# Optimization experiments

Hardware: AMD Instinct MI355X
Metric: run time of the kernel (lower is better)

Reference implementation:

```python
import jax, jax.numpy as jnp
import numpy as np

NP = 4            # num_patches
P = NP * NP       # num_patches^2
BIG = 1e8         # self-distance sentinel used by the torch module
IN_CH = 128
MID = IN_CH // 2
NUM_CONVS = 3
KS = 3
B, H, W = 4, 256, 256


def conv2d(x, w, b):
    # x: [B,C,H,W], w: [O,I,kh,kw] (OIHW), stride 1, 'same' padding
    pad = (w.shape[-1] - 1) // 2
    y = jax.lax.conv_general_dilated(
        x, w, window_strides=(1, 1), padding=[(pad, pad), (pad, pad)],
        dimension_numbers=('NCHW', 'OIHW', 'NCHW'))
    return y + b[None, :, None, None]


def patchify(x):
    # [B,C,H,W] -> [B,P,C,hs,ws] with row-major patch order (i*NP+j)
    b, c, h, w = x.shape
    hs, ws = h // NP, w // NP
    x = x.reshape(b, c, NP, hs, NP, ws).transpose(0, 2, 4, 1, 3, 5)
    return x.reshape(b, P, c, hs, ws)


def unpatchify(xp, h, w):
    b, p, c, hs, ws = xp.shape
    x = xp.reshape(b, NP, NP, c, hs, ws).transpose(0, 3, 1, 4, 2, 5)
    return x.reshape(b, c, h, w)


def setup_inputs() -> dict:
    key = jax.random.key(0)
    ks = jax.random.split(key, 16)
    s = 0.05  # weight init scale (~kaiming for these fan-ins)
    inp = {
        'x':     jax.random.normal(ks[0], (B, IN_CH, H, W), jnp.float32),
        'pre_w': jax.random.normal(ks[1], (MID, IN_CH, KS, KS), jnp.float32) * s,
        'pre_b': jnp.zeros((MID,), jnp.float32),
        'c1_w':  jax.random.normal(ks[2], (NUM_CONVS, MID, MID, KS, KS), jnp.float32) * s,
        'c1_b':  jnp.zeros((NUM_CONVS, MID), jnp.float32),
        'c2_w':  jax.random.normal(ks[3], (NUM_CONVS, MID, MID, KS, KS), jnp.float32) * s,
        'c2_b':  jnp.zeros((NUM_CONVS, MID), jnp.float32),
        'p1_w':  jax.random.normal(ks[4], (P, MID, MID), jnp.float32) * s,  # [patch, out, in] 1x1 conv
        'p1_b':  jnp.zeros((P, MID), jnp.float32),
        'p2_w':  jax.random.normal(ks[5], (P, MID, MID), jnp.float32) * s,
        'p2_b':  jnp.zeros((P, MID), jnp.float32),
        'fin_w': jax.random.normal(ks[6], (IN_CH, IN_CH, KS, KS), jnp.float32) * s,
        'fin_b': jnp.zeros((IN_CH,), jnp.float32),
    }
    return inp


def reference(x, pre_w, pre_b, c1_w, c1_b, c2_w, c2_b,
              p1_w, p1_b, p2_w, p2_b, fin_w, fin_b):
    x0 = jax.nn.relu(conv2d(x, pre_w, pre_b))
    h1 = x0
    for i in range(c1_w.shape[0]):
        h1 = jax.nn.relu(conv2d(h1, c1_w[i], c1_b[i]))
    x1 = h1 + x0
    h2 = x0
    for i in range(c2_w.shape[0]):
        h2 = jax.nn.relu(conv2d(h2, c2_w[i], c2_b[i]))
    x2 = h2 + x0

    # per-patch 1x1 convs (all P patches batched via einsum)
    x1p = patchify(x1)  # [B,P,C,hs,ws]
    x2p = patchify(x2)
    x1p = jnp.einsum('bpchw,pdc->bpdhw', x1p, p1_w) + p1_b[None, :, :, None, None]
    x2p = jnp.einsum('bpchw,pdc->bpdhw', x2p, p2_w) + p2_b[None, :, :, None, None]

    # pairwise squared distances between x1 patches and x2 patches
    f1 = x1p.reshape(B, P, -1)
    f2 = x2p.reshape(B, P, -1)
    d = ((f1 ** 2).sum(-1)[:, :, None]
         + (f2 ** 2).sum(-1)[:, None, :]
         - 2.0 * jnp.einsum('bpd,bqd->bpq', f1, f2))  # [B,P,P]
    d = jnp.where(jnp.eye(P, dtype=bool)[None], BIG, d)
    # torch does softmax(exp(-d)) — keep the double transform faithfully
    attn = jax.nn.softmax(jnp.exp(-d), axis=-1)  # [B,P,P]

    outp = jnp.einsum('bpq,bqchw->bpchw', attn, x2p)
    out = unpatchify(outp, H, W)           # [B,MID,H,W]
    out = jnp.concatenate([out, x0], axis=1)  # [B,IN_CH,H,W]
    out = jax.nn.relu(conv2d(out, fin_w, fin_b))
    return out + x
```

## Files before the change

### kernel.cpp

```cpp
#include <hip/hip_runtime.h>
#include <hip/hip_bf16.h>

#define BB   4
#define HH   256
#define WW   256
#define INCH 128
#define MIDC 64
#define NPAT 4
#define PP   16
#define PS   64

typedef __bf16 bf16x8 __attribute__((ext_vector_type(8)));
typedef float f32x4 __attribute__((ext_vector_type(4)));
typedef unsigned short ushort_t;

#define UPL 16777216UL

__device__ inline ushort_t f2bf(float f) {
    unsigned u = __float_as_uint(f);
    unsigned r = (u + 0x7FFFu + ((u >> 16) & 1u)) >> 16;
    return (ushort_t)r;
}
__device__ inline float bf2f(ushort_t h) {
    return __uint_as_float(((unsigned)h) << 16);
}
__device__ inline f32x4 mfma16(uint4 a, uint4 b, f32x4 c) {
    return __builtin_amdgcn_mfma_f32_16x16x32_bf16(
        __builtin_bit_cast(bf16x8, a), __builtin_bit_cast(bf16x8, b), c, 0, 0, 0);
}

__global__ __launch_bounds__(256) void setup_kernel(
    const float* __restrict__ x,     ushort_t* __restrict__ xh,
    const float* __restrict__ pre_w, const float* __restrict__ c1_w,
    const float* __restrict__ c2_w,  const float* __restrict__ fin_w,
    const float* __restrict__ p1_w,  const float* __restrict__ p2_w,
    const float* __restrict__ c1_b,  const float* __restrict__ c2_b,
    ushort_t* __restrict__ wpPre, ushort_t* __restrict__ wpC,
    ushort_t* __restrict__ wpFin, ushort_t* __restrict__ pw1b,
    ushort_t* __restrict__ pw2b,  float* __restrict__ zbuf,
    float* __restrict__ cbias)
{
    __shared__ ushort_t sm[64 * 136];
    const int t = threadIdx.x;
    const int bx = blockIdx.x;
    if (bx < 4096) {
        const int b = bx >> 10;
        const int pxbase = (bx & 1023) * 64;
#pragma unroll
        for (int i = 0; i < 32; ++i) {
            int idx = i * 256 + t;
            int c = idx >> 6, pxl = idx & 63;
            sm[pxl * 136 + c] = f2bf(x[((size_t)(b * 128 + c)) * 65536 + pxbase + pxl]);
        }
        __syncthreads();
#pragma unroll
        for (int i = 0; i < 4; ++i) {
            int idx = i * 256 + t;
            int pxl = idx >> 4, q = idx & 15;
            uint4 v = *(const uint4*)&sm[pxl * 136 + q * 8];
            *(uint4*)(xh + ((size_t)b * 65536 + pxbase + pxl) * 128 + q * 8) = v;
        }
        return;
    }
    int idx = (bx - 4096) * 256 + t;
    if (idx < 73728) {
        int tap = idx % 9, ci = (idx / 9) % 128, co = idx / 1152;
        wpPre[(tap * 64 + co) * 128 + ci] = f2bf(pre_w[idx]);
    } else if (idx < 294912) {
        int j = idx - 73728;
        int which = j / 36864, k = j % 36864;
        const float* src = (which < 3) ? (c1_w + (size_t)which * 36864)
                                       : (c2_w + (size_t)(which - 3) * 36864);
        int tap = k % 9, ci = (k / 9) % 64, co = k / 576;
        wpC[(size_t)which * 36864 + (tap * 64 + co) * 64 + ci] = f2bf(src[k]);
    } else if (idx < 442368) {
        int k = idx - 294912;
        int tap = k % 9, ci = (k / 9) % 128, co = k / 1152;
        wpFin[(tap * 128 + co) * 128 + ci] = f2bf(fin_w[k]);
    } else if (idx < 507904) {
        pw1b[idx - 442368] = f2bf(p1_w[idx - 442368]);
    } else if (idx < 573440) {
        pw2b[idx - 507904] = f2bf(p2_w[idx - 507904]);
    } else if (idx < 574592) {
        zbuf[idx - 573440] = 0.f;
    } else if (idx < 574784) {
        cbias[idx - 574592] = c1_b[idx - 574592];
    } else if (idx < 574976) {
        cbias[192 + idx - 574784] = c2_b[idx - 574784];
    }
}

template<int CIN, int CSPLIT>
__device__ inline void stage10x34(const ushort_t* inA, const ushort_t* inB,
                                  int b, int y0, int x0, int t, int cb,
                                  uint4 (&stg)[6])
{
#pragma unroll
    for (int i = 0; i < 6; ++i) {
        int e = i * 256 + t;
        int pxl = e >> 2, quad = e & 3;
        int row = pxl / 34, xl = pxl - row * 34;
        int gy = y0 + row - 1, gx = x0 + xl - 1;
        bool ok = (e < 1360) && ((unsigned)gy < 256u) && ((unsigned)gx < 256u);
        int c0 = cb + quad * 8;
        const ushort_t* src; int nch, ch;
        if ((CSPLIT == CIN) || (c0 < CSPLIT)) { src = inA; nch = CSPLIT; ch = c0; }
        else { src = inB; nch = CIN - CSPLIT; ch = c0 - CSPLIT; }
        uint4 v = make_uint4(0u, 0u, 0u, 0u);
        if (ok) v = *(const uint4*)(src + ((size_t)((b * 256 + gy) * 256 + gx)) * nch + ch);
        stg[i] = v;
    }
}

template<int CIN, int CSPLIT>
__device__ inline void stage6x68(const ushort_t* inA, const ushort_t* inB,
                                 int b, int y0, int x0, int t, int cb,
                                 uint4 (&stg)[7])
{
#pragma unroll
    for (int i = 0; i < 7; ++i) {
        int e = i * 256 + t;
        int pxl = e >> 2, quad = e & 3;
        int row = pxl / 68, xl = pxl - row * 68;
        int gy = y0 + row - 1, gx = x0 + xl - 1;
        bool ok = (e < 1632) && ((unsigned)gy < 256u) && ((unsigned)gx < 256u);
        int c0 = cb + quad * 8;
        const ushort_t* src; int nch, ch;
        if ((CSPLIT == CIN) || (c0 < CSPLIT)) { src = inA; nch = CSPLIT; ch = c0; }
        else { src = inB; nch = CIN - CSPLIT; ch = c0 - CSPLIT; }
        uint4 v = make_uint4(0u, 0u, 0u, 0u);
        if (ok) v = *(const uint4*)(src + ((size_t)((b * 256 + gy) * 256 + gx)) * nch + ch);
        stg[i] = v;
    }
}

template<int CIN, int CSPLIT, int OMODE, bool PAIR>
__global__ __launch_bounds__(256) void mconv3x3(
    const ushort_t* __restrict__ inA, const ushort_t* __restrict__ inB,
    const ushort_t* __restrict__ wgtT,
    const float* __restrict__ bias,
    const void* __restrict__ res,
    void* __restrict__ out,
    int COUT, size_t inStride, size_t wStride, size_t bStride, size_t outStride)
{
    constexpr int NCH = CIN / 32;
    __shared__ ushort_t sm[10 * 34 * 36];

    const int t = threadIdx.x;
    const int nx = gridDim.x;
    const int bid = blockIdx.x;
    const int fid = (bid & 7) * (nx >> 3) + (bid >> 3);
    const int tile = fid;
    const int cog = PAIR ? 0 : blockIdx.y * 64;
    const int y0 = (tile >> 3) * 8;
    const int x0 = (tile & 7) * 32;
    const int br = PAIR ? blockIdx.y : 0;
    const ushort_t* inAb = inA + (size_t)br * inStride;
    const ushort_t* inBb = inB + (size_t)br * inStride;
    const ushort_t* wgt  = wgtT + (size_t)br * wStride;
    const float*    bs   = bias + (size_t)br * bStride;
    const int b = blockIdx.z;
    const int l = t & 63, w = t >> 6;
    const int lan15 = l & 15;
    const int g4 = l >> 4;
    const int k8 = g4 * 8;
    const int co0 = cog + (w & 1) * 32;
    const int xw = (w >> 1) * 16;

    f32x4 acc[2][8];
#pragma unroll
    for (int mt = 0; mt < 2; ++mt)
#pragma unroll
        for (int r = 0; r < 8; ++r) acc[mt][r] = (f32x4)0.f;

    uint4 stg[6];
    stage10x34<CIN, CSPLIT>(inAb, inBb, b, y0, x0, t, 0, stg);

    for (int cc = 0; cc < NCH; ++cc) {
        __syncthreads();
#pragma unroll
        for (int i = 0; i < 6; ++i) {
            int e = i * 256 + t;
            if (e < 1360) {
                int pxl = e >> 2, quad = e & 3;
                *(uint4*)&sm[pxl * 36 + quad * 8] = stg[i];
            }
        }
        __syncthreads();
        if (cc + 1 < NCH)
            stage10x34<CIN, CSPLIT>(inAb, inBb, b, y0, x0, t, (cc + 1) * 32, stg);

        const int cb = cc * 32;
        uint4 af[2][9];
#pragma unroll
        for (int mt = 0; mt < 2; ++mt)
#pragma unroll
            for (int tap = 0; tap < 9; ++tap)
                af[mt][tap] = *(const uint4*)(wgt +
                    ((size_t)tap * COUT + co0 + mt * 16 + lan15) * CIN + cb + k8);

#pragma unroll
        for (int s = 0; s < 10; ++s) {
#pragma unroll
            for (int dx = 0; dx < 3; ++dx) {
                const int pxl = s * 34 + xw + lan15 + dx;
                uint4 bv = *(const uint4*)&sm[pxl * 36 + k8];
#pragma unroll
                for (int dy = 0; dy < 3; ++dy) {
                    const int r = s - dy;
                    if (r >= 0 && r < 8) {
                        acc[0][r] = mfma16(af[0][dy * 3 + dx], bv, acc[0][r]);
                        acc[1][r] = mfma16(af[1][dy * 3 + dx], bv, acc[1][r]);
                    }
                }
            }
        }
    }

#pragma unroll
    for (int mt = 0; mt < 2; ++mt) {
#pragma unroll
        for (int r = 0; r < 8; ++r) {
            const int y = y0 + r;
            const int x = x0 + xw + lan15;
            const int codr = co0 + mt * 16 + g4 * 4;
            float v[4];
#pragma unroll
            for (int j = 0; j < 4; ++j)
                v[j] = fmaxf(acc[mt][r][j] + bs[codr + j], 0.f);
            const size_t pix = (size_t)(b * 256 + y) * 256 + x;
            if constexpr (OMODE == 1) {
                const ushort_t* rp = (const ushort_t*)res + pix * 64 + codr;
#pragma unroll
                for (int j = 0; j < 4; ++j) v[j] += bf2f(rp[j]);
            }
            uint2 pk;
            pk.x = (unsigned)f2bf(v[0]) | ((unsigned)f2bf(v[1]) << 16);
            pk.y = (unsigned)f2bf(v[2]) | ((unsigned)f2bf(v[3]) << 16);
            *(uint2*)((ushort_t*)out + (size_t)br * outStride + pix * COUT + codr) = pk;
        }
    }
}

template<int CIN, int CSPLIT, int OMODE, bool COPAIR>
__global__ __launch_bounds__(256) void wconv3x3(
    const ushort_t* __restrict__ inA, const ushort_t* __restrict__ inB,
    const ushort_t* __restrict__ wgtT,
    const float* __restrict__ bias,
    const void* __restrict__ res,
    void* __restrict__ out,
    int COUT)
{
    constexpr int NCH = CIN / 32;
    __shared__ ushort_t sm[6 * 68 * 32];

    const int t = threadIdx.x;
    const int nx = gridDim.x;
    const int bid = blockIdx.x;
    const int fid = (bid & 7) * (nx >> 3) + (bid >> 3);
    int tile, cog;
    if (COPAIR) { tile = fid >> 1; cog = (fid & 1) * 64; }
    else        { tile = fid;      cog = blockIdx.y * 64; }
    const int y0 = (tile >> 2) * 4;
    const int x0 = (tile & 3) * 64;
    const int b = blockIdx.z;
    const int l = t & 63, w = t >> 6;
    const int lan15 = l & 15;
    const int g4 = l >> 4;
    const int k8 = g4 * 8;
    const int co0 = cog + (w & 1) * 32;
    const int wrow0 = (w >> 1) * 2;

    f32x4 acc[2][8];
#pragma unroll
    for (int mt = 0; mt < 2; ++mt)
#pragma unroll
        for (int nt = 0; nt < 8; ++nt) acc[mt][nt] = (f32x4)0.f;

    uint4 stg[7];
    stage6x68<CIN, CSPLIT>(inA, inB, b, y0, x0, t, 0, stg);

    for (int cc = 0; cc < NCH; ++cc) {
        __syncthreads();
#pragma unroll
        for (int i = 0; i < 7; ++i) {
            int e = i * 256 + t;
            if (e < 1632) {
                int pxl = e >> 2, quad = e & 3;
                *(uint4*)&sm[pxl * 32 + quad * 8] = stg[i];
            }
        }
        __syncthreads();
        if (cc + 1 < NCH)
            stage6x68<CIN, CSPLIT>(inA, inB, b, y0, x0, t, (cc + 1) * 32, stg);

        const int cb = cc * 32;
        uint4 af[2][9];
#pragma unroll
        for (int mt = 0; mt < 2; ++mt)
#pragma unroll
            for (int tap = 0; tap < 9; ++tap)
                af[mt][tap] = *(const uint4*)(wgtT +
                    ((size_t)tap * COUT + co0 + mt * 16 + lan15) * CIN + cb + k8);

#pragma unroll
        for (int rr = 0; rr < 4; ++rr) {
            const int r = wrow0 + rr;
#pragma unroll
            for (int col = 0; col < 4; ++col) {
#pragma unroll
                for (int dx = 0; dx < 3; ++dx) {
                    const int xc = col * 16 + lan15 + dx;
                    uint4 bv = *(const uint4*)&sm[(r * 68 + xc) * 32 + k8];
#pragma unroll
                    for (int drow = 0; drow < 2; ++drow) {
                        const int dy = rr - drow;
                        if (dy >= 0 && dy < 3) {
                            const int tap = dy * 3 + dx;
                            const int nt = drow * 4 + col;
                            acc[0][nt] = mfma16(af[0][tap], bv, acc[0][nt]);
                            acc[1][nt] = mfma16(af[1][tap], bv, acc[1][nt]);
                        }
                    }
                }
            }
        }
    }

#pragma unroll
    for (int mt = 0; mt < 2; ++mt) {
#pragma unroll
        for (int nt = 0; nt < 8; ++nt) {
            const int y = y0 + wrow0 + (nt >> 2);
            const int x = x0 + (nt & 3) * 16 + lan15;
            const int codr = co0 + mt * 16 + g4 * 4;
            float v[4];
#pragma unroll
            for (int j = 0; j < 4; ++j)
                v[j] = fmaxf(acc[mt][nt][j] + bias[codr + j], 0.f);
            if constexpr (OMODE == 2) {
                const float* rf = (const float*)res;
                float* of = (float*)out;
#pragma unroll
                for (int j = 0; j < 4; ++j) {
                    size_t oi = ((size_t)(b * COUT + codr + j) * 256 + y) * 256 + x;
                    of[oi] = v[j] + rf[oi];
                }
            } else {
                const size_t pix = (size_t)(b * 256 + y) * 256 + x;
                uint2 pk;
                pk.x = (unsigned)f2bf(v[0]) | ((unsigned)f2bf(v[1]) << 16);
                pk.y = (unsigned)f2bf(v[2]) | ((unsigned)f2bf(v[3]) << 16);
                *(uint2*)((ushort_t*)out + pix * COUT + codr) = pk;
            }
        }
    }
}

__global__ __launch_bounds__(256) void patch1x1_mfma(
    const ushort_t* __restrict__ in0, const ushort_t* __restrict__ pwb0,
    const float* __restrict__ bias1, const float* __restrict__ bias2,
    ushort_t* __restrict__ outp0, float* __restrict__ nrm0)
{
    __shared__ ushort_t smp[256 * 72];
    const int side = blockIdx.z;
    const ushort_t* in  = in0  + (size_t)side * UPL;
    const ushort_t* pwb = pwb0 + side * 65536;
    const float*   bias = side ? bias2 : bias1;
    ushort_t*      outp = outp0 + (size_t)side * UPL;
    float*         nrm  = nrm0 + side * 64;

    const int t = threadIdx.x;
    const int bx = blockIdx.x;
    const int bp = blockIdx.y;
    const int b = bp >> 4, p = bp & 15;
    const int py = (p >> 2) * 64, px0 = (p & 3) * 64;
    const int l = t & 63, w = t >> 6;
    const int lan15 = l & 15, k8 = (l >> 4) * 8;

#pragma unroll
    for (int i = 0; i < 8; ++i) {
        int idx = i * 256 + t;
        int px = idx >> 3, q = idx & 7;
        int y = py + bx * 4 + (px >> 6), x = px0 + (px & 63);
        uint4 v = *(const uint4*)(in + ((size_t)(b * 256 + y) * 256 + x) * 64 + q * 8);
        *(uint4*)&smp[px * 72 + q * 8] = v;
    }
    __syncthreads();

    uint4 af[4][2];
#pragma unroll
    for (int mt = 0; mt < 4; ++mt)
#pragma unroll
        for (int kk = 0; kk < 2; ++kk)
            af[mt][kk] = *(const uint4*)(pwb + (size_t)p * 4096 +
                                         (mt * 16 + lan15) * 64 + kk * 32 + k8);

    f32x4 acc[4][4];
#pragma unroll
    for (int mt = 0; mt < 4; ++mt)
#pragma unroll
        for (int j = 0; j < 4; ++j) acc[mt][j] = (f32x4)0.f;

#pragma unroll
    for (int kk = 0; kk < 2; ++kk)
#pragma unroll
        for (int j = 0; j < 4; ++j) {
            int px = (w * 4 + j) * 16 + lan15;
            uint4 bv = *(const uint4*)&smp[px * 72 + kk * 32 + k8];
#pragma unroll
            for (int mt = 0; mt < 4; ++mt)
                acc[mt][j] = mfma16(af[mt][kk], bv, acc[mt][j]);
        }

    float nsum = 0.f;
#pragma unroll
    for (int mt = 0; mt < 4; ++mt)
#pragma unroll
        for (int j = 0; j < 4; ++j) {
            int px = (w * 4 + j) * 16 + lan15;
            int y = py + bx * 4 + (px >> 6), x = px0 + (px & 63);
            int d0 = mt * 16 + (l >> 4) * 4;
            float v[4];
#pragma unroll
            for (int r = 0; r < 4; ++r) {
                v[r] = acc[mt][j][r] + bias[p * 64 + d0 + r];
                nsum = fmaf(v[r], v[r], nsum);
            }
            uint2 pk;
            pk.x = (unsigned)f2bf(v[0]) | ((unsigned)f2bf(v[1]) << 16);
            pk.y = (unsigned)f2bf(v[2]) | ((unsigned)f2bf(v[3]) << 16);
            *(uint2*)(outp + ((size_t)(b * 256 + y) * 256 + x) * 64 + d0) = pk;
        }

#pragma unroll
    for (int off = 32; off > 0; off >>= 1) nsum += __shfl_down(nsum, off);
    if (l == 0) atomicAdd(&nrm[b * 16 + p], nsum);
}

__global__ __launch_bounds__(256) void patch_dots_mfma(
    const ushort_t* __restrict__ f1, const ushort_t* __restrict__ f2,
    float* __restrict__ dotv)
{
    __shared__ float rbuf[4][64][4];
    const int t = threadIdx.x;
    const int kb = blockIdx.x;
    const int b = blockIdx.y;
    const int l = t & 63, w = t >> 6;
    const int lan15 = l & 15, k8q = (l >> 4) * 8;
    const int p = lan15;
    const int py = (p >> 2) * 64, px0 = (p & 3) * 64;
    const size_t rowbase = ((size_t)(b * 256 + py + kb) * 256 + px0) * 64;

    f32x4 acc = (f32x4)0.f;
    for (int ixl = 0; ixl < 16; ++ixl) {
        const size_t pa = rowbase + (size_t)(w * 16 + ixl) * 64 + k8q;
#pragma unroll
        for (int c0 = 0; c0 < 64; c0 += 32) {
            uint4 av = *(const uint4*)(f1 + pa + c0);
            uint4 bv = *(const uint4*)(f2 + pa + c0);
            acc = mfma16(av, bv, acc);
        }
    }
#pragma unroll
    for (int r = 0; r < 4; ++r) rbuf[w][l][r] = acc[r];
    __syncthreads();
    if (t < 64) {
#pragma unroll
        for (int r = 0; r < 4; ++r) {
            float s = rbuf[0][t][r] + rbuf[1][t][r] + rbuf[2][t][r] + rbuf[3][t][r];
            int pp = (t >> 4) * 4 + r, qq = t & 15;
            atomicAdd(&dotv[b * 256 + pp * 16 + qq], s);
        }
    }
}

__global__ __launch_bounds__(1024) void attn_kernel(
    const float* __restrict__ n1, const float* __restrict__ n2,
    const float* __restrict__ dotv, float* __restrict__ attn)
{
    __shared__ float tv[1024];
    int t = threadIdx.x;
    int b = t >> 8, p = (t >> 4) & 15, q = t & 15;
    float d = n1[b * 16 + p] + n2[b * 16 + q] - 2.f * dotv[t];
    if (p == q) d = 1e8f;
    float e = expf(-d);
    tv[t] = e;
    __syncthreads();
    const float* row = &tv[(t >> 4) << 4];
    float m = row[0];
#pragma unroll
    for (int j = 1; j < 16; ++j) m = fmaxf(m, row[j]);
    float ssum = 0.f;
#pragma unroll
    for (int j = 0; j < 16; ++j) ssum += expf(row[j] - m);
    attn[t] = expf(e - m) / ssum;
}

__global__ __launch_bounds__(256) void combine_kernel(
    const float* __restrict__ attn, const ushort_t* __restrict__ x2p,
    ushort_t* __restrict__ cmb)
{
    int gid = blockIdx.x * 256 + threadIdx.x;
    int cq = gid & 7;
    int pxg = (gid >> 3) & 65535;
    int b = gid >> 19;
    int y = pxg >> 8, x = pxg & 255;
    int p = (y >> 6) * 4 + (x >> 6);
    int i = y & 63, j = x & 63;
    const float* arow = attn + (size_t)(b * 16 + p) * 16;
    float s[8];
#pragma unroll
    for (int k = 0; k < 8; ++k) s[k] = 0.f;
#pragma unroll
    for (int q = 0; q < 16; ++q) {
        float a = arow[q];
        const ushort_t* sp = x2p +
            ((size_t)(b * 256 + (q >> 2) * 64 + i) * 256 + (q & 3) * 64 + j) * 64 + cq * 8;
        uint4 v = *(const uint4*)sp;
        unsigned uu[4] = {v.x, v.y, v.z, v.w};
#pragma unroll
        for (int h = 0; h < 4; ++h) {
            s[h * 2]     = fmaf(a, bf2f((ushort_t)(uu[h] & 0xffffu)), s[h * 2]);
            s[h * 2 + 1] = fmaf(a, bf2f((ushort_t)(uu[h] >> 16)),     s[h * 2 + 1]);
        }
    }
    uint4 o;
    o.x = (unsigned)f2bf(s[0]) | ((unsigned)f2bf(s[1]) << 16);
    o.y = (unsigned)f2bf(s[2]) | ((unsigned)f2bf(s[3]) << 16);
    o.z = (unsigned)f2bf(s[4]) | ((unsigned)f2bf(s[5]) << 16);
    o.w = (unsigned)f2bf(s[6]) | ((unsigned)f2bf(s[7]) << 16);
    *(uint4*)(cmb + ((size_t)b * 65536 + pxg) * 64 + cq * 8) = o;
}

extern "C" void kernel_launch(void* const* d_in, const int* in_sizes, int n_in,
                              void* d_out, int out_size, void* d_ws, size_t ws_size,
                              hipStream_t stream)
{
    const float* x     = (const float*)d_in[0];
    const float* pre_w = (const float*)d_in[1];
    const float* pre_b = (const float*)d_in[2];
    const float* c1_w  = (const float*)d_in[3];
    const float* c1_b  = (const float*)d_in[4];
    const float* c2_w  = (const float*)d_in[5];
    const float* c2_b  = (const float*)d_in[6];
    const float* p1_w  = (const float*)d_in[7];
    const float* p1_b  = (const float*)d_in[8];
    const float* p2_w  = (const float*)d_in[9];
    const float* p2_b  = (const float*)d_in[10];
    const float* fin_w = (const float*)d_in[11];
    const float* fin_b = (const float*)d_in[12];

    float* out = (float*)d_out;
    ushort_t* wsu = (ushort_t*)d_ws;

    const size_t U = UPL;

    ushort_t* xh   = wsu;
    ushort_t* x0b  = wsu + 2 * U;
    ushort_t* tA   = wsu;
    ushort_t* tB   = wsu + 3 * U;
    ushort_t* x12b = (ushort_t*)d_out;
    ushort_t* x1p  = tB;
    ushort_t* x2p  = tB + U;
    ushort_t* cmb  = wsu;

    ushort_t* wpPre = wsu + 5 * U;
    ushort_t* wpC   = wpPre + 73728;
    ushort_t* wpFin = wpC + 6 * 36864;
    ushort_t* pw1b  = wpFin + 147456;
    ushort_t* pw2b  = pw1b + 65536;
    float* n1    = (float*)(pw2b + 65536);
    float* n2    = n1 + 64;
    float* dotv  = n2 + 64;
    float* attn  = dotv + 1024;
    float* cbias = attn + 1024;

    const dim3 blk(256);

    setup_kernel<<<4096 + (574976 + 255) / 256, blk, 0, stream>>>(
        x, xh, pre_w, c1_w, c2_w, fin_w, p1_w, p2_w, c1_b, c2_b,
        wpPre, wpC, wpFin, pw1b, pw2b, n1, cbias);

    const dim3 gWide(256, 1, BB);
    const dim3 gPair(256, 2, BB);
    const dim3 gFin(512, 1, BB);

    wconv3x3<128, 128, 0, false><<<gWide, blk, 0, stream>>>(
        xh, xh, wpPre, pre_b, nullptr, x0b, 64);

    mconv3x3<64, 64, 0, true><<<gPair, blk, 0, stream>>>(
        x0b, x0b, wpC, cbias, nullptr, tA, 64,
        0, 3 * 36864, 192, U);
    mconv3x3<64, 64, 0, true><<<gPair, blk, 0, stream>>>(
        tA, tA, wpC + 36864, cbias + 64, nullptr, tB, 64,
        U, 3 * 36864, 192, U);
    mconv3x3<64, 64, 1, true><<<gPair, blk, 0, stream>>>(
        tB, tB, wpC + 2 * 36864, cbias + 128, x0b, x12b, 64,
        U, 3 * 36864, 192, U);

    const dim3 pgrid(16, BB * PP, 2);
    patch1x1_mfma<<<pgrid, blk, 0, stream>>>(x12b, pw1b, p1_b, p2_b, x1p, n1);

    const dim3 dgrid(64, BB);
    patch_dots_mfma<<<dgrid, blk, 0, stream>>>(x1p, x2p, dotv);

    attn_kernel<<<1, 1024, 0, stream>>>(n1, n2, dotv, attn);

    combine_kernel<<<BB * 65536 * 8 / 256, blk, 0, stream>>>(attn, x2p, cmb);

    wconv3x3<128, 64, 2, true><<<gFin, blk, 0, stream>>>(
        cmb, x0b, wpFin, fin_b, x, out, 128);
}
```

Measured before the change: 535.1 us.

## Stage conv input halos directly into LDS via global_load_lds

Replaces the register-staged global-to-LDS copy in both 3x3 MFMA conv kernels with direct global_load_lds transfers, zero-filling out-of-bounds halo entries only on border tiles. The conv_10x34 LDS row stride drops from 36 to 32 elements to match the contiguous layout the direct loads produce. This removes the staging registers and VGPR-to-LDS stores, but also removes the software prefetch of the next channel chunk, so each chunk's load is now exposed before compute. The unpadded stride may also add LDS bank conflicts on the B-fragment reads.

```diff
diff --git a/kernel.cpp b/kernel.cpp
--- a/kernel.cpp
+++ b/kernel.cpp
@@ -13,6 +13,8 @@
 typedef __bf16 bf16x8 __attribute__((ext_vector_type(8)));
 typedef float f32x4 __attribute__((ext_vector_type(4)));
 typedef unsigned short ushort_t;
+typedef const __attribute__((address_space(1))) void gvoid_t;
+typedef __attribute__((address_space(3))) void lvoid_t;
 
 #define UPL 16777216UL
 
@@ -91,10 +93,23 @@
 }
 
 template<int CIN, int CSPLIT>
-__device__ inline void stage10x34(const ushort_t* inA, const ushort_t* inB,
-                                  int b, int y0, int x0, int t, int cb,
-                                  uint4 (&stg)[6])
-{
+__device__ inline void stage10x34_lds(const ushort_t* inA, const ushort_t* inB,
+                                      int b, int y0, int x0, int t, int cb,
+                                      ushort_t* sm, bool border)
+{
+    if (border) {
+#pragma unroll
+        for (int i = 0; i < 6; ++i) {
+            int e = i * 256 + t;
+            if (e < 1360) {
+                int pxl = e >> 2;
+                int row = pxl / 34, xl = pxl - row * 34;
+                int gy = y0 + row - 1, gx = x0 + xl - 1;
+                if (!(((unsigned)gy < 256u) && ((unsigned)gx < 256u)))
+                    *(uint4*)&sm[(size_t)e * 8] = make_uint4(0u, 0u, 0u, 0u);
+            }
+        }
+    }
 #pragma unroll
     for (int i = 0; i < 6; ++i) {
         int e = i * 256 + t;
@@ -106,17 +121,31 @@
         const ushort_t* src; int nch, ch;
         if ((CSPLIT == CIN) || (c0 < CSPLIT)) { src = inA; nch = CSPLIT; ch = c0; }
         else { src = inB; nch = CIN - CSPLIT; ch = c0 - CSPLIT; }
-        uint4 v = make_uint4(0u, 0u, 0u, 0u);
-        if (ok) v = *(const uint4*)(src + ((size_t)((b * 256 + gy) * 256 + gx)) * nch + ch);
-        stg[i] = v;
+        const ushort_t* gp = src + ((size_t)((b * 256 + gy) * 256 + gx)) * nch + ch;
+        ushort_t* lp = sm + ((size_t)(i * 256 + (t & 192))) * 8;
+        if (ok)
+            __builtin_amdgcn_global_load_lds((gvoid_t*)gp, (lvoid_t*)lp, 16, 0, 0);
     }
 }
 
 template<int CIN, int CSPLIT>
-__device__ inline void stage6x68(const ushort_t* inA, const ushort_t* inB,
-                                 int b, int y0, int x0, int t, int cb,
-                                 uint4 (&stg)[7])
-{
+__device__ inline void stage6x68_lds(const ushort_t* inA, const ushort_t* inB,
+                                     int b, int y0, int x0, int t, int cb,
+                                     ushort_t* sm, bool border)
+{
+    if (border) {
+#pragma unroll
+        for (int i = 0; i < 7; ++i) {
+            int e = i * 256 + t;
+            if (e < 1632) {
+                int pxl = e >> 2;
+                int row = pxl / 68, xl = pxl - row * 68;
+                int gy = y0 + row - 1, gx = x0 + xl - 1;
+                if (!(((unsigned)gy < 256u) && ((unsigned)gx < 256u)))
+                    *(uint4*)&sm[(size_t)e * 8] = make_uint4(0u, 0u, 0u, 0u);
+            }
+        }
+    }
 #pragma unroll
     for (int i = 0; i < 7; ++i) {
         int e = i * 256 + t;
@@ -128,9 +157,10 @@
         const ushort_t* src; int nch, ch;
         if ((CSPLIT == CIN) || (c0 < CSPLIT)) { src = inA; nch = CSPLIT; ch = c0; }
         else { src = inB; nch = CIN - CSPLIT; ch = c0 - CSPLIT; }
-        uint4 v = make_uint4(0u, 0u, 0u, 0u);
-        if (ok) v = *(const uint4*)(src + ((size_t)((b * 256 + gy) * 256 + gx)) * nch + ch);
-        stg[i] = v;
+        const ushort_t* gp = src + ((size_t)((b * 256 + gy) * 256 + gx)) * nch + ch;
+        ushort_t* lp = sm + ((size_t)(i * 256 + (t & 192))) * 8;
+        if (ok)
+            __builtin_amdgcn_global_load_lds((gvoid_t*)gp, (lvoid_t*)lp, 16, 0, 0);
     }
 }
 
@@ -144,7 +174,7 @@
     int COUT, size_t inStride, size_t wStride, size_t bStride, size_t outStride)
 {
     constexpr int NCH = CIN / 32;
-    __shared__ ushort_t sm[10 * 34 * 36];
+    __shared__ ushort_t sm[10 * 34 * 32];
 
     const int t = threadIdx.x;
     const int nx = gridDim.x;
@@ -154,6 +184,7 @@
     const int cog = PAIR ? 0 : blockIdx.y * 64;
     const int y0 = (tile >> 3) * 8;
     const int x0 = (tile & 7) * 32;
+    const bool border = (y0 == 0) | (y0 == 248) | (x0 == 0) | (x0 == 224);
     const int br = PAIR ? blockIdx.y : 0;
     const ushort_t* inAb = inA + (size_t)br * inStride;
     const ushort_t* inBb = inB + (size_t)br * inStride;
@@ -173,22 +204,10 @@
 #pragma unroll
         for (int r = 0; r < 8; ++r) acc[mt][r] = (f32x4)0.f;
 
-    uint4 stg[6];
-    stage10x34<CIN, CSPLIT>(inAb, inBb, b, y0, x0, t, 0, stg);
-
     for (int cc = 0; cc < NCH; ++cc) {
+        if (cc) __syncthreads();
+        stage10x34_lds<CIN, CSPLIT>(inAb, inBb, b, y0, x0, t, cc * 32, sm, border);
         __syncthreads();
-#pragma unroll
-        for (int i = 0; i < 6; ++i) {
-            int e = i * 256 + t;
-            if (e < 1360) {
-                int pxl = e >> 2, quad = e & 3;
-                *(uint4*)&sm[pxl * 36 + quad * 8] = stg[i];
-            }
-        }
-        __syncthreads();
-        if (cc + 1 < NCH)
-            stage10x34<CIN, CSPLIT>(inAb, inBb, b, y0, x0, t, (cc + 1) * 32, stg);
 
         const int cb = cc * 32;
         uint4 af[2][9];
@@ -204,7 +223,7 @@
 #pragma unroll
             for (int dx = 0; dx < 3; ++dx) {
                 const int pxl = s * 34 + xw + lan15 + dx;
-                uint4 bv = *(const uint4*)&sm[pxl * 36 + k8];
+                uint4 bv = *(const uint4*)&sm[pxl * 32 + k8];
 #pragma unroll
                 for (int dy = 0; dy < 3; ++dy) {
                     const int r = s - dy;
@@ -263,6 +282,7 @@
     else        { tile = fid;      cog = blockIdx.y * 64; }
     const int y0 = (tile >> 2) * 4;
     const int x0 = (tile & 3) * 64;
+    const bool border = (y0 == 0) | (y0 == 252) | (x0 == 0) | (x0 == 192);
     const int b = blockIdx.z;
     const int l = t & 63, w = t >> 6;
     const int lan15 = l & 15;
@@ -277,22 +297,10 @@
 #pragma unroll
         for (int nt = 0; nt < 8; ++nt) acc[mt][nt] = (f32x4)0.f;
 
-    uint4 stg[7];
-    stage6x68<CIN, CSPLIT>(inA, inB, b, y0, x0, t, 0, stg);
-
     for (int cc = 0; cc < NCH; ++cc) {
+        if (cc) __syncthreads();
+        stage6x68_lds<CIN, CSPLIT>(inA, inB, b, y0, x0, t, cc * 32, sm, border);
         __syncthreads();
-#pragma unroll
-        for (int i = 0; i < 7; ++i) {
-            int e = i * 256 + t;
-            if (e < 1632) {
-                int pxl = e >> 2, quad = e & 3;
-                *(uint4*)&sm[pxl * 32 + quad * 8] = stg[i];
-            }
-        }
-        __syncthreads();
-        if (cc + 1 < NCH)
-            stage6x68<CIN, CSPLIT>(inA, inB, b, y0, x0, t, (cc + 1) * 32, stg);
 
         const int cb = cc * 32;
         uint4 af[2][9];
```

Measured after the change: 540.4 us. About the same (+1.0%).

## Stream wconv3x3 input tiles directly into double-buffered LDS via global_load_lds

Applied to the files above, without the earlier changes.

The wide 3x3 conv kernel now uses async global-to-LDS loads (global_load_lds) instead of staging each input chunk through registers and then writing it to shared memory. The shared tile is double-buffered so the next channel chunk loads while MFMAs run on the current one. This removes one barrier per chunk and frees the staging registers. Out-of-bounds halo entries are zeroed once, and only on border tiles. LDS use doubles, which may cut occupancy, and correctness depends on the barrier waiting for the async LDS writes.

```diff
diff --git a/kernel.cpp b/kernel.cpp
--- a/kernel.cpp
+++ b/kernel.cpp
@@ -13,6 +13,8 @@
 typedef __bf16 bf16x8 __attribute__((ext_vector_type(8)));
 typedef float f32x4 __attribute__((ext_vector_type(4)));
 typedef unsigned short ushort_t;
+typedef const __attribute__((address_space(1))) void gvoid_t;
+typedef __attribute__((address_space(3))) void lvoid_t;
 
 #define UPL 16777216UL
 
@@ -112,10 +114,25 @@
     }
 }
 
+__device__ inline void zero6x68_oob(ushort_t* sm, int y0, int x0, int t)
+{
+#pragma unroll
+    for (int i = 0; i < 7; ++i) {
+        int e = i * 256 + t;
+        if (e < 1632) {
+            int pxl = e >> 2;
+            int row = pxl / 68, xl = pxl - row * 68;
+            int gy = y0 + row - 1, gx = x0 + xl - 1;
+            if (!(((unsigned)gy < 256u) && ((unsigned)gx < 256u)))
+                *(uint4*)&sm[(size_t)e * 8] = make_uint4(0u, 0u, 0u, 0u);
+        }
+    }
+}
+
 template<int CIN, int CSPLIT>
-__device__ inline void stage6x68(const ushort_t* inA, const ushort_t* inB,
-                                 int b, int y0, int x0, int t, int cb,
-                                 uint4 (&stg)[7])
+__device__ inline void load6x68_lds(const ushort_t* inA, const ushort_t* inB,
+                                    int b, int y0, int x0, int t, int cb,
+                                    ushort_t* sm)
 {
 #pragma unroll
     for (int i = 0; i < 7; ++i) {
@@ -128,9 +145,10 @@
         const ushort_t* src; int nch, ch;
         if ((CSPLIT == CIN) || (c0 < CSPLIT)) { src = inA; nch = CSPLIT; ch = c0; }
         else { src = inB; nch = CIN - CSPLIT; ch = c0 - CSPLIT; }
-        uint4 v = make_uint4(0u, 0u, 0u, 0u);
-        if (ok) v = *(const uint4*)(src + ((size_t)((b * 256 + gy) * 256 + gx)) * nch + ch);
-        stg[i] = v;
+        const ushort_t* gp = src + ((size_t)((b * 256 + gy) * 256 + gx)) * nch + ch;
+        ushort_t* lp = sm + ((size_t)(i * 256 + (t & 192))) * 8;
+        if (ok)
+            __builtin_amdgcn_global_load_lds((gvoid_t*)gp, (lvoid_t*)lp, 16, 0, 0);
     }
 }
 
@@ -252,7 +270,7 @@
     int COUT)
 {
     constexpr int NCH = CIN / 32;
-    __shared__ ushort_t sm[6 * 68 * 32];
+    __shared__ ushort_t sm[2][6 * 68 * 32];
 
     const int t = threadIdx.x;
     const int nx = gridDim.x;
@@ -263,6 +281,7 @@
     else        { tile = fid;      cog = blockIdx.y * 64; }
     const int y0 = (tile >> 2) * 4;
     const int x0 = (tile & 3) * 64;
+    const bool border = (y0 == 0) | (y0 == 252) | (x0 == 0) | (x0 == 192);
     const int b = blockIdx.z;
     const int l = t & 63, w = t >> 6;
     const int lan15 = l & 15;
@@ -277,22 +296,18 @@
 #pragma unroll
         for (int nt = 0; nt < 8; ++nt) acc[mt][nt] = (f32x4)0.f;
 
-    uint4 stg[7];
-    stage6x68<CIN, CSPLIT>(inA, inB, b, y0, x0, t, 0, stg);
+    if (border) {
+        zero6x68_oob(sm[0], y0, x0, t);
+        zero6x68_oob(sm[1], y0, x0, t);
+    }
+    load6x68_lds<CIN, CSPLIT>(inA, inB, b, y0, x0, t, 0, sm[0]);
 
     for (int cc = 0; cc < NCH; ++cc) {
         __syncthreads();
-#pragma unroll
-        for (int i = 0; i < 7; ++i) {
-            int e = i * 256 + t;
-            if (e < 1632) {
-                int pxl = e >> 2, quad = e & 3;
-                *(uint4*)&sm[pxl * 32 + quad * 8] = stg[i];
-            }
-        }
-        __syncthreads();
         if (cc + 1 < NCH)
-            stage6x68<CIN, CSPLIT>(inA, inB, b, y0, x0, t, (cc + 1) * 32, stg);
+            load6x68_lds<CIN, CSPLIT>(inA, inB, b, y0, x0, t, (cc + 1) * 32,
+                                      sm[(cc + 1) & 1]);
+        const ushort_t* smc = sm[cc & 1];
 
         const int cb = cc * 32;
         uint4 af[2][9];
@@ -311,7 +326,7 @@
 #pragma unroll
                 for (int dx = 0; dx < 3; ++dx) {
                     const int xc = col * 16 + lan15 + dx;
-                    uint4 bv = *(const uint4*)&sm[(r * 68 + xc) * 32 + k8];
+                    uint4 bv = *(const uint4*)&smc[(r * 68 + xc) * 32 + k8];
 #pragma unroll
                     for (int drow = 0; drow < 2; ++drow) {
                         const int dy = rr - drow;
```

Result: no change. 535.3 us (+0.0%).

## Switch wide 3x3 convs to 32x32x16 MFMA tiles with padded LDS rows

Applied to the files above, without the earlier changes.

The pre-conv and final 3x3 conv kernels are rewritten to use 32x32x16 bf16 MFMA instead of 16x16x32. Each wave now computes a 64-output-channel by 2-row by 32-pixel tile, loading each input row once per dx and reusing it across the three dy taps. LDS pixel stride is padded from 32 to 36 halfwords to reduce bank conflicts. The intent is fewer LDS reads and fewer MFMA issues per unit of work, at the cost of a different output write pattern and larger accumulator register use.

```diff
diff --git a/kernel.cpp b/kernel.cpp
--- a/kernel.cpp
+++ b/kernel.cpp
@@ -12,6 +12,7 @@
 
 typedef __bf16 bf16x8 __attribute__((ext_vector_type(8)));
 typedef float f32x4 __attribute__((ext_vector_type(4)));
+typedef float f32x16 __attribute__((ext_vector_type(16)));
 typedef unsigned short ushort_t;
 
 #define UPL 16777216UL
@@ -26,6 +27,10 @@
 }
 __device__ inline f32x4 mfma16(uint4 a, uint4 b, f32x4 c) {
     return __builtin_amdgcn_mfma_f32_16x16x32_bf16(
+        __builtin_bit_cast(bf16x8, a), __builtin_bit_cast(bf16x8, b), c, 0, 0, 0);
+}
+__device__ inline f32x16 mfma32(uint4 a, uint4 b, f32x16 c) {
+    return __builtin_amdgcn_mfma_f32_32x32x16_bf16(
         __builtin_bit_cast(bf16x8, a), __builtin_bit_cast(bf16x8, b), c, 0, 0, 0);
 }
 
@@ -243,7 +248,7 @@
 }
 
 template<int CIN, int CSPLIT, int OMODE, bool COPAIR>
-__global__ __launch_bounds__(256) void wconv3x3(
+__global__ __launch_bounds__(256) void wconv32(
     const ushort_t* __restrict__ inA, const ushort_t* __restrict__ inB,
     const ushort_t* __restrict__ wgtT,
     const float* __restrict__ bias,
@@ -252,7 +257,7 @@
     int COUT)
 {
     constexpr int NCH = CIN / 32;
-    __shared__ ushort_t sm[6 * 68 * 32];
+    __shared__ ushort_t sm[6 * 68 * 36];
 
     const int t = threadIdx.x;
     const int nx = gridDim.x;
@@ -265,17 +270,16 @@
     const int x0 = (tile & 3) * 64;
     const int b = blockIdx.z;
     const int l = t & 63, w = t >> 6;
-    const int lan15 = l & 15;
-    const int g4 = l >> 4;
-    const int k8 = g4 * 8;
-    const int co0 = cog + (w & 1) * 32;
-    const int wrow0 = (w >> 1) * 2;
-
-    f32x4 acc[2][8];
-#pragma unroll
-    for (int mt = 0; mt < 2; ++mt)
-#pragma unroll
-        for (int nt = 0; nt < 8; ++nt) acc[mt][nt] = (f32x4)0.f;
+    const int l31 = l & 31;
+    const int khi = l >> 5;
+    const int pr = w & 1;
+    const int xh = w >> 1;
+
+    f32x16 acc[2][2];
+#pragma unroll
+    for (int m = 0; m < 2; ++m)
+#pragma unroll
+        for (int o = 0; o < 2; ++o) acc[m][o] = (f32x16)0.f;
 
     uint4 stg[7];
     stage6x68<CIN, CSPLIT>(inA, inB, b, y0, x0, t, 0, stg);
@@ -287,71 +291,73 @@
             int e = i * 256 + t;
             if (e < 1632) {
                 int pxl = e >> 2, quad = e & 3;
-                *(uint4*)&sm[pxl * 32 + quad * 8] = stg[i];
+                *(uint4*)&sm[pxl * 36 + quad * 8] = stg[i];
             }
         }
         __syncthreads();
         if (cc + 1 < NCH)
             stage6x68<CIN, CSPLIT>(inA, inB, b, y0, x0, t, (cc + 1) * 32, stg);
 
-        const int cb = cc * 32;
-        uint4 af[2][9];
-#pragma unroll
-        for (int mt = 0; mt < 2; ++mt)
-#pragma unroll
-            for (int tap = 0; tap < 9; ++tap)
-                af[mt][tap] = *(const uint4*)(wgtT +
-                    ((size_t)tap * COUT + co0 + mt * 16 + lan15) * CIN + cb + k8);
-
-#pragma unroll
-        for (int rr = 0; rr < 4; ++rr) {
-            const int r = wrow0 + rr;
-#pragma unroll
-            for (int col = 0; col < 4; ++col) {
-#pragma unroll
-                for (int dx = 0; dx < 3; ++dx) {
-                    const int xc = col * 16 + lan15 + dx;
-                    uint4 bv = *(const uint4*)&sm[(r * 68 + xc) * 32 + k8];
-#pragma unroll
-                    for (int drow = 0; drow < 2; ++drow) {
-                        const int dy = rr - drow;
-                        if (dy >= 0 && dy < 3) {
-                            const int tap = dy * 3 + dx;
-                            const int nt = drow * 4 + col;
-                            acc[0][nt] = mfma16(af[0][tap], bv, acc[0][nt]);
-                            acc[1][nt] = mfma16(af[1][tap], bv, acc[1][nt]);
-                        }
-                    }
+#pragma unroll
+        for (int kk = 0; kk < 2; ++kk) {
+            const int cbk = cc * 32 + kk * 16;
+            uint4 af[2][9];
+#pragma unroll
+            for (int m = 0; m < 2; ++m)
+#pragma unroll
+                for (int tap = 0; tap < 9; ++tap)
+                    af[m][tap] = *(const uint4*)(wgtT +
+                        ((size_t)tap * COUT + cog + m * 32 + l31) * CIN + cbk + khi * 8);
+
+#pragma unroll
+            for (int dx = 0; dx < 3; ++dx) {
+                uint4 bv[4];
+#pragma unroll
+                for (int ir = 0; ir < 4; ++ir) {
+                    const int pxl = (pr * 2 + ir) * 68 + xh * 32 + l31 + dx;
+                    bv[ir] = *(const uint4*)&sm[pxl * 36 + kk * 16 + khi * 8];
+                }
+#pragma unroll
+                for (int dy = 0; dy < 3; ++dy) {
+                    const int tap = dy * 3 + dx;
+#pragma unroll
+                    for (int o = 0; o < 2; ++o)
+#pragma unroll
+                        for (int m = 0; m < 2; ++m)
+                            acc[m][o] = mfma32(af[m][tap], bv[o + dy], acc[m][o]);
                 }
             }
         }
     }
 
 #pragma unroll
-    for (int mt = 0; mt < 2; ++mt) {
-#pragma unroll
-        for (int nt = 0; nt < 8; ++nt) {
-            const int y = y0 + wrow0 + (nt >> 2);
-            const int x = x0 + (nt & 3) * 16 + lan15;
-            const int codr = co0 + mt * 16 + g4 * 4;
-            float v[4];
-#pragma unroll
-            for (int j = 0; j < 4; ++j)
-                v[j] = fmaxf(acc[mt][nt][j] + bias[codr + j], 0.f);
-            if constexpr (OMODE == 2) {
-                const float* rf = (const float*)res;
-                float* of = (float*)out;
-#pragma unroll
-                for (int j = 0; j < 4; ++j) {
-                    size_t oi = ((size_t)(b * COUT + codr + j) * 256 + y) * 256 + x;
-                    of[oi] = v[j] + rf[oi];
+    for (int m = 0; m < 2; ++m) {
+#pragma unroll
+        for (int o = 0; o < 2; ++o) {
+            const int y = y0 + pr * 2 + o;
+            const int x = x0 + xh * 32 + l31;
+            const size_t pix = (size_t)(b * 256 + y) * 256 + x;
+#pragma unroll
+            for (int q = 0; q < 4; ++q) {
+                const int co = cog + m * 32 + q * 8 + khi * 4;
+                float v[4];
+#pragma unroll
+                for (int rr = 0; rr < 4; ++rr)
+                    v[rr] = fmaxf(acc[m][o][q * 4 + rr] + bias[co + rr], 0.f);
+                if constexpr (OMODE == 2) {
+                    const float* rf = (const float*)res;
+                    float* of = (float*)out;
+#pragma unroll
+                    for (int rr = 0; rr < 4; ++rr) {
+                        size_t oi = ((size_t)(b * COUT + co + rr) * 256 + y) * 256 + x;
+                        of[oi] = v[rr] + rf[oi];
+                    }
+                } else {
+                    uint2 pk;
+                    pk.x = (unsigned)f2bf(v[0]) | ((unsigned)f2bf(v[1]) << 16);
+                    pk.y = (unsigned)f2bf(v[2]) | ((unsigned)f2bf(v[3]) << 16);
+                    *(uint2*)((ushort_t*)out + pix * COUT + co) = pk;
                 }
-            } else {
-                const size_t pix = (size_t)(b * 256 + y) * 256 + x;
-                uint2 pk;
-                pk.x = (unsigned)f2bf(v[0]) | ((unsigned)f2bf(v[1]) << 16);
-                pk.y = (unsigned)f2bf(v[2]) | ((unsigned)f2bf(v[3]) << 16);
-                *(uint2*)((ushort_t*)out + pix * COUT + codr) = pk;
             }
         }
     }
@@ -586,7 +592,7 @@
     const dim3 gPair(256, 2, BB);
     const dim3 gFin(512, 1, BB);
 
-    wconv3x3<128, 128, 0, false><<<gWide, blk, 0, stream>>>(
+    wconv32<128, 128, 0, false><<<gWide, blk, 0, stream>>>(
         xh, xh, wpPre, pre_b, nullptr, x0b, 64);
 
     mconv3x3<64, 64, 0, true><<<gPair, blk, 0, stream>>>(
@@ -609,6 +615,6 @@
 
     combine_kernel<<<BB * 65536 * 8 / 256, blk, 0, stream>>>(attn, x2p, cmb);
 
-    wconv3x3<128, 64, 2, true><<<gFin, blk, 0, stream>>>(
+    wconv32<128, 64, 2, true><<<gFin, blk, 0, stream>>>(
         cmb, x0b, wpFin, fin_b, x, out, 128);
 }
```

Result: slower. 616.6 us (+15.2%).
